# Optimization experiments

Hardware: AMD Instinct MI355X
Metric: run time of the kernel (lower is better)

## Reference

```python
import jax, jax.numpy as jnp
import numpy as np

B, N, E, H = 8, 2048, 1024, 16
D = E // H

def setup_inputs() -> dict:
    key = jax.random.key(0)
    kx, kw1, kb1, kw2, kb2 = jax.random.split(key, 5)
    scale = 0.02
    return {
        "x": jax.random.normal(kx, (B, N, E), dtype=jnp.float32),
        "Wqkv": jax.random.normal(kw1, (3 * E, E), dtype=jnp.float32) * scale,
        "bqkv": jax.random.normal(kb1, (3 * E,), dtype=jnp.float32) * scale,
        "Wo": jax.random.normal(kw2, (E, E), dtype=jnp.float32) * scale,
        "bo": jax.random.normal(kb2, (E,), dtype=jnp.float32) * scale,
    }

def reference(x, Wqkv, bqkv, Wo, bo):
    b, n, e = x.shape
    h, d = H, D
    # qkv projection: torch Linear is x @ W.T + b
    qkv = x @ Wqkv.T + bqkv                                   # [B,N,3E]
    qkv = qkv.reshape(b, n, 3, h, d).transpose(2, 0, 3, 1, 4)  # [3,B,H,N,D]
    q, k, v = qkv[0], qkv[1], qkv[2]                           # each [B,H,N,D]
    # NOTE: replicates the original's einsum labeling exactly: with q,k of
    # shape [B,H,N,D], 'nqhd,nkhd->nhqk' contracts over D and yields [B,N,H,H]
    # (softmax over the head axis), matching the torch source bit-for-bit.
    energy = jnp.einsum('nqhd,nkhd->nhqk', q, k)               # [B,N,H,H]
    attention = jax.nn.softmax(energy / jnp.sqrt(jnp.float32(e)), axis=-1)
    out = jnp.einsum('nhql,nlhd->nqhd', attention, v)          # [B,H,N,D]
    out = out.reshape(b, n, e)                                 # same raw-buffer reshape as torch
    return out @ Wo.T + bo
```

## Files before the change

### kernel.cpp

```cpp
#include <hip/hip_runtime.h>
#include <hip/hip_bf16.h>
#include <stdint.h>


typedef __attribute__((ext_vector_type(8))) short short8;
typedef __attribute__((ext_vector_type(8))) unsigned short ushort8;
typedef __attribute__((ext_vector_type(4))) float floatx4;

__device__ __forceinline__ unsigned short f2bf(float f) {
  union { float f; uint32_t u; } x; x.f = f;
  uint32_t u = x.u;
  return (unsigned short)((u + 0x7fffu + ((u >> 16) & 1u)) >> 16);
}
__device__ __forceinline__ float bf2f(unsigned short s) {
  union { uint32_t u; float f; } x; x.u = ((uint32_t)s) << 16; return x.f;
}
__device__ __forceinline__ void unpack8(uint4 u, float* f) {
  f[0] = bf2f((unsigned short)(u.x & 0xffffu)); f[1] = bf2f((unsigned short)(u.x >> 16));
  f[2] = bf2f((unsigned short)(u.y & 0xffffu)); f[3] = bf2f((unsigned short)(u.y >> 16));
  f[4] = bf2f((unsigned short)(u.z & 0xffffu)); f[5] = bf2f((unsigned short)(u.z >> 16));
  f[6] = bf2f((unsigned short)(u.w & 0xffffu)); f[7] = bf2f((unsigned short)(u.w >> 16));
}

__global__ __launch_bounds__(256) void cvt_all(const float* __restrict__ x,
                                               const float* __restrict__ w1,
                                               const float* __restrict__ w2,
                                               unsigned short* __restrict__ xb,
                                               unsigned short* __restrict__ w1b,
                                               unsigned short* __restrict__ w2b) {
  int i = blockIdx.x * 256 + threadIdx.x;
  const float* src;
  unsigned short* dst;
  if (i < 2097152) {
    src = x; dst = xb;
  } else if (i < 2097152 + 393216) {
    i -= 2097152; src = w1; dst = w1b;
  } else {
    i -= 2490368; src = w2; dst = w2b;
  }
  long base = (long)i * 8;
  const float4* p = (const float4*)(src + base);
  float4 a = p[0], b = p[1];
  ushort8 r;
  r[0] = f2bf(a.x); r[1] = f2bf(a.y); r[2] = f2bf(a.z); r[3] = f2bf(a.w);
  r[4] = f2bf(b.x); r[5] = f2bf(b.y); r[6] = f2bf(b.z); r[7] = f2bf(b.w);
  *(ushort8*)(dst + base) = r;
}

__device__ __forceinline__ void gl2lds16(const void* g, void* l) {
  __builtin_amdgcn_global_load_lds(
      (const uint32_t __attribute__((address_space(1)))*)g,
      (uint32_t __attribute__((address_space(3)))*)(uint32_t)(uintptr_t)l,
      16, 0, 0);
}

template <bool OUT_BF16>
__device__ __forceinline__ void gemm256_core(const unsigned short* __restrict__ A,
                                             const unsigned short* __restrict__ Bm,
                                             const float* __restrict__ bias,
                                             void* __restrict__ Cout,
                                             int K, int ncols, int ldc) {
  __shared__ __align__(16) char lds[131072];
  char* lA = lds;
  char* lB = lds + 65536;

  const int id = blockIdx.x;
  const int local = id % (8 * ncols);
  const int brow = (id / (8 * ncols)) * 8 + (local & 7);
  const int bcol = local >> 3;
  const long row0 = (long)brow * 256;
  const long col0 = (long)bcol * 256;

  const int tid = threadIdx.x;
  const int lane = tid & 63;
  const int wave = tid >> 6;
  const int wm = wave >> 2;
  const int wn = wave & 3;
  const int l15 = lane & 15;
  const int lk = lane >> 4;

  float bv[4];
#pragma unroll
  for (int n = 0; n < 4; ++n) bv[n] = bias[col0 + wn * 64 + n * 16 + l15];
  asm volatile("s_waitcnt vmcnt(0)" ::: "memory");

  const int trow = tid >> 2;
  const int gch = (tid & 3) ^ ((tid >> 3) & 3);
  const unsigned short* gA = A + (row0 + trow) * (long)K + gch * 8;
  const unsigned short* gB = Bm + (col0 + trow) * (long)K + gch * 8;
  const long rstep = (long)128 * K;
  char* dA = lA + tid * 16;
  char* dB = lB + tid * 16;

  const int ch = ((lk ^ ((l15 >> 1) & 3)) << 4);
  const int aoff = (wm * 128 + l15) * 64 + ch;
  const int boff = (wn * 64 + l15) * 64 + ch;

  floatx4 acc[8][4] = {};
  const int NT = K >> 5;

#pragma unroll
  for (int t = 0; t < 3; ++t) {
    const long ko = (long)t * 32;
    gl2lds16(gA + ko, dA + t * 16384);
    gl2lds16(gA + rstep + ko, dA + t * 16384 + 8192);
    gl2lds16(gB + ko, dB + t * 16384);
    gl2lds16(gB + rstep + ko, dB + t * 16384 + 8192);
  }
  asm volatile("s_waitcnt vmcnt(8)" ::: "memory");
  __builtin_amdgcn_s_barrier();

#pragma unroll 1
  for (int kt = 0; kt < NT; ++kt) {
    const char* bufA = lA + (kt & 3) * 16384;
    const char* bufB = lB + (kt & 3) * 16384;
    const bool stage = (kt + 3 < NT);
    const long ko = (long)(kt + 3) * 32;
    const int sb = ((kt + 3) & 3) * 16384;

    short8 af[8], bfr[4];
#pragma unroll
    for (int n = 0; n < 4; ++n) bfr[n] = *(const short8*)(bufB + boff + n * 1024);
    af[0] = *(const short8*)(bufA + aoff + 0 * 1024);
    af[1] = *(const short8*)(bufA + aoff + 1 * 1024);
    af[2] = *(const short8*)(bufA + aoff + 2 * 1024);
    af[3] = *(const short8*)(bufA + aoff + 3 * 1024);
    asm volatile("s_waitcnt lgkmcnt(2)" ::: "memory");
    __builtin_amdgcn_sched_barrier(0);
    __builtin_amdgcn_s_setprio(1);
#pragma unroll
    for (int n = 0; n < 4; ++n) {
      acc[0][n] = __builtin_amdgcn_mfma_f32_16x16x32_bf16(af[0], bfr[n], acc[0][n], 0, 0, 0);
      acc[1][n] = __builtin_amdgcn_mfma_f32_16x16x32_bf16(af[1], bfr[n], acc[1][n], 0, 0, 0);
    }
    __builtin_amdgcn_s_setprio(0);
    af[4] = *(const short8*)(bufA + aoff + 4 * 1024);
    af[5] = *(const short8*)(bufA + aoff + 5 * 1024);
    asm volatile("s_waitcnt lgkmcnt(2)" ::: "memory");
    __builtin_amdgcn_sched_barrier(0);
    __builtin_amdgcn_s_setprio(1);
#pragma unroll
    for (int n = 0; n < 4; ++n) {
      acc[2][n] = __builtin_amdgcn_mfma_f32_16x16x32_bf16(af[2], bfr[n], acc[2][n], 0, 0, 0);
      acc[3][n] = __builtin_amdgcn_mfma_f32_16x16x32_bf16(af[3], bfr[n], acc[3][n], 0, 0, 0);
    }
    __builtin_amdgcn_s_setprio(0);
    af[6] = *(const short8*)(bufA + aoff + 6 * 1024);
    af[7] = *(const short8*)(bufA + aoff + 7 * 1024);
    if (stage) {
      gl2lds16(gA + ko, dA + sb);
      gl2lds16(gA + rstep + ko, dA + sb + 8192);
      gl2lds16(gB + ko, dB + sb);
      gl2lds16(gB + rstep + ko, dB + sb + 8192);
    }
    asm volatile("s_waitcnt lgkmcnt(2)" ::: "memory");
    __builtin_amdgcn_sched_barrier(0);
    __builtin_amdgcn_s_setprio(1);
#pragma unroll
    for (int n = 0; n < 4; ++n) {
      acc[4][n] = __builtin_amdgcn_mfma_f32_16x16x32_bf16(af[4], bfr[n], acc[4][n], 0, 0, 0);
      acc[5][n] = __builtin_amdgcn_mfma_f32_16x16x32_bf16(af[5], bfr[n], acc[5][n], 0, 0, 0);
    }
    __builtin_amdgcn_s_setprio(0);
    asm volatile("s_waitcnt lgkmcnt(0)" ::: "memory");
    __builtin_amdgcn_sched_barrier(0);
    __builtin_amdgcn_s_setprio(1);
#pragma unroll
    for (int n = 0; n < 4; ++n) {
      acc[6][n] = __builtin_amdgcn_mfma_f32_16x16x32_bf16(af[6], bfr[n], acc[6][n], 0, 0, 0);
      acc[7][n] = __builtin_amdgcn_mfma_f32_16x16x32_bf16(af[7], bfr[n], acc[7][n], 0, 0, 0);
    }
    __builtin_amdgcn_s_setprio(0);
    __builtin_amdgcn_sched_barrier(0);
    if (kt < NT - 3) { asm volatile("s_waitcnt vmcnt(8)" ::: "memory"); }
    else if (kt == NT - 3) { asm volatile("s_waitcnt vmcnt(4)" ::: "memory"); }
    else if (kt == NT - 2) { asm volatile("s_waitcnt vmcnt(0)" ::: "memory"); }
    __builtin_amdgcn_s_barrier();
  }

  const long crow0 = row0 + wm * 128 + lk * 4;
  const long ccol0 = col0 + wn * 64 + l15;
#pragma unroll
  for (int m = 0; m < 8; ++m)
#pragma unroll
    for (int n = 0; n < 4; ++n)
#pragma unroll
      for (int r = 0; r < 4; ++r) {
        const long row = crow0 + m * 16 + r;
        const long col = ccol0 + n * 16;
        const float v = acc[m][n][r] + bv[n];
        if (OUT_BF16)
          ((unsigned short*)Cout)[row * ldc + col] = f2bf(v);
        else
          ((float*)Cout)[row * ldc + col] = v;
      }
}

__global__ __launch_bounds__(512, 2) void gemm_qkv(const unsigned short* __restrict__ A,
                                                   const unsigned short* __restrict__ Bm,
                                                   const float* __restrict__ bias,
                                                   unsigned short* __restrict__ Cout, int K) {
  gemm256_core<true>(A, Bm, bias, Cout, K, 12, 3072);
}
__global__ __launch_bounds__(512, 2) void gemm_out(const unsigned short* __restrict__ A,
                                                   const unsigned short* __restrict__ Bm,
                                                   const float* __restrict__ bias,
                                                   float* __restrict__ Cout, int K) {
  gemm256_core<false>(A, Bm, bias, Cout, K, 4, 1024);
}

__global__ __launch_bounds__(256) void attn_kernel(const unsigned short* __restrict__ qkv,
                                                   unsigned short* __restrict__ out2) {
  __shared__ __align__(16) char lds[4 * 6144];
  const int tid = threadIdx.x;
  const int wave = tid >> 6;
  const int lane = tid & 63;
  const int token = blockIdx.x * 4 + wave;
  const int head = lane >> 2;
  const int sub = lane & 3;
  const int b = token >> 11;
  const int s = token & 2047;

  const char* gbase = (const char*)qkv + (long)token * 6144;
  char* lbase = lds + wave * 6144;
#pragma unroll
  for (int p = 0; p < 6; p++)
    gl2lds16(gbase + p * 1024 + lane * 16, lbase + p * 1024 + lane * 16);
  __syncthreads();

  float qf[16];
  {
    const uint4* qp = (const uint4*)(lbase + head * 128 + sub * 32);
    unpack8(qp[0], qf);
    unpack8(qp[1], qf + 8);
  }

  float e[16];
  const char* kbase = lbase + 2048 + sub * 32;
  for (int j = 0; j < 16; j++) {
    const uint4* kp = (const uint4*)(kbase + j * 128);
    float kf[16];
    unpack8(kp[0], kf);
    unpack8(kp[1], kf + 8);
    float a0 = 0.f, a1 = 0.f, a2 = 0.f, a3 = 0.f;
#pragma unroll
    for (int c = 0; c < 4; c++) {
      a0 += qf[c] * kf[c];
      a1 += qf[c + 4] * kf[c + 4];
      a2 += qf[c + 8] * kf[c + 8];
      a3 += qf[c + 12] * kf[c + 12];
    }
    float ej = (a0 + a1) + (a2 + a3);
    ej += __shfl_xor(ej, 1);
    ej += __shfl_xor(ej, 2);
    e[j] = ej * 0.03125f;
  }

  float mx = e[0];
#pragma unroll
  for (int j = 1; j < 16; j++) mx = fmaxf(mx, e[j]);
  float sum = 0.f;
#pragma unroll
  for (int j = 0; j < 16; j++) { e[j] = __expf(e[j] - mx); sum += e[j]; }
  const float inv = 1.f / sum;

  float o[16];
#pragma unroll
  for (int d = 0; d < 16; d++) o[d] = 0.f;
  const char* vbase = lbase + 4096 + sub * 32;
  for (int j = 0; j < 16; j++) {
    const float wgt = e[j] * inv;
    const uint4* vp = (const uint4*)(vbase + j * 128);
    float vf[16];
    unpack8(vp[0], vf);
    unpack8(vp[1], vf + 8);
#pragma unroll
    for (int d = 0; d < 16; d++) o[d] += wgt * vf[d];
  }

  const long row = (long)b * 2048 + head * 128 + (s >> 4);
  unsigned short* op = out2 + row * 1024 + (long)(s & 15) * 64 + sub * 16;
#pragma unroll
  for (int w = 0; w < 2; w++) {
    ushort8 r;
#pragma unroll
    for (int c = 0; c < 8; c++) r[c] = f2bf(o[w * 8 + c]);
    *(ushort8*)(op + w * 8) = r;
  }
}

extern "C" void kernel_launch(void* const* d_in, const int* in_sizes, int n_in,
                              void* d_out, int out_size, void* d_ws, size_t ws_size,
                              hipStream_t stream) {
  const float* x    = (const float*)d_in[0];
  const float* Wqkv = (const float*)d_in[1];
  const float* bqkv = (const float*)d_in[2];
  const float* Wo   = (const float*)d_in[3];
  const float* bo   = (const float*)d_in[4];
  float* out = (float*)d_out;

  char* ws = (char*)d_ws;
  unsigned short* x_bf    = (unsigned short*)(ws);
  unsigned short* wqkv_bf = (unsigned short*)(ws + 33554432);
  unsigned short* wo_bf   = (unsigned short*)(ws + 39845888);
  unsigned short* qkv_bf  = (unsigned short*)(ws + 41943040);
  unsigned short* out2_bf = (unsigned short*)(ws + 142606336);

  cvt_all<<<10240, 256, 0, stream>>>(x, Wqkv, Wo, x_bf, wqkv_bf, wo_bf);

  gemm_qkv<<<64 * 12, 512, 0, stream>>>(x_bf, wqkv_bf, bqkv, qkv_bf, 1024);

  attn_kernel<<<4096, 256, 0, stream>>>(qkv_bf, out2_bf);

  gemm_out<<<64 * 4, 512, 0, stream>>>(out2_bf, wo_bf, bo, out, 1024);
}
```

Baseline: 316.0 us.

## Compute head-mixing attention with bf16 MFMA and XOR-swizzled LDS layout

Replaces the scalar per-lane dot products and weighted sums in the attention kernel with 16x16x32 bf16 MFMA instructions for both QK^T and attention×V. An XOR swizzle is applied when staging qkv rows into LDS to avoid bank conflicts on the transposed reads. Attention probabilities are now rounded to bf16 before the PV product, which adds precision loss. The V operand is gathered with scalar 16-bit LDS reads, and half the MFMA K dimension is zero-padded.

```diff
diff --git a/kernel.cpp b/kernel.cpp
--- a/kernel.cpp
+++ b/kernel.cpp
@@ -5,21 +5,13 @@
 
 typedef __attribute__((ext_vector_type(8))) short short8;
 typedef __attribute__((ext_vector_type(8))) unsigned short ushort8;
+typedef __attribute__((ext_vector_type(4))) unsigned short ushort4v;
 typedef __attribute__((ext_vector_type(4))) float floatx4;
 
 __device__ __forceinline__ unsigned short f2bf(float f) {
   union { float f; uint32_t u; } x; x.f = f;
   uint32_t u = x.u;
   return (unsigned short)((u + 0x7fffu + ((u >> 16) & 1u)) >> 16);
-}
-__device__ __forceinline__ float bf2f(unsigned short s) {
-  union { uint32_t u; float f; } x; x.u = ((uint32_t)s) << 16; return x.f;
-}
-__device__ __forceinline__ void unpack8(uint4 u, float* f) {
-  f[0] = bf2f((unsigned short)(u.x & 0xffffu)); f[1] = bf2f((unsigned short)(u.x >> 16));
-  f[2] = bf2f((unsigned short)(u.y & 0xffffu)); f[3] = bf2f((unsigned short)(u.y >> 16));
-  f[4] = bf2f((unsigned short)(u.z & 0xffffu)); f[5] = bf2f((unsigned short)(u.z >> 16));
-  f[6] = bf2f((unsigned short)(u.w & 0xffffu)); f[7] = bf2f((unsigned short)(u.w >> 16));
 }
 
 __global__ __launch_bounds__(256) void cvt_all(const float* __restrict__ x,
@@ -216,76 +208,82 @@
   const int wave = tid >> 6;
   const int lane = tid & 63;
   const int token = blockIdx.x * 4 + wave;
-  const int head = lane >> 2;
-  const int sub = lane & 3;
+  const int l15 = lane & 15;
+  const int lk = lane >> 4;
   const int b = token >> 11;
   const int s = token & 2047;
 
   const char* gbase = (const char*)qkv + (long)token * 6144;
   char* lbase = lds + wave * 6144;
 #pragma unroll
-  for (int p = 0; p < 6; p++)
-    gl2lds16(gbase + p * 1024 + lane * 16, lbase + p * 1024 + lane * 16);
+  for (int p = 0; p < 6; p++) {
+    const int o = p * 1024 + lane * 16;
+    const int row = o >> 7;
+    const int chs = ((o >> 4) & 7) ^ (row & 7);
+    const int src = (o & ~127) | (chs << 4);
+    gl2lds16(gbase + src, lbase + o);
+  }
   __syncthreads();
 
-  float qf[16];
-  {
-    const uint4* qp = (const uint4*)(lbase + head * 128 + sub * 32);
-    unpack8(qp[0], qf);
-    unpack8(qp[1], qf + 8);
-  }
-
-  float e[16];
-  const char* kbase = lbase + 2048 + sub * 32;
-  for (int j = 0; j < 16; j++) {
-    const uint4* kp = (const uint4*)(kbase + j * 128);
-    float kf[16];
-    unpack8(kp[0], kf);
-    unpack8(kp[1], kf + 8);
-    float a0 = 0.f, a1 = 0.f, a2 = 0.f, a3 = 0.f;
-#pragma unroll
-    for (int c = 0; c < 4; c++) {
-      a0 += qf[c] * kf[c];
-      a1 += qf[c + 4] * kf[c + 4];
-      a2 += qf[c + 8] * kf[c + 8];
-      a3 += qf[c + 12] * kf[c + 12];
-    }
-    float ej = (a0 + a1) + (a2 + a3);
-    ej += __shfl_xor(ej, 1);
-    ej += __shfl_xor(ej, 2);
-    e[j] = ej * 0.03125f;
-  }
-
-  float mx = e[0];
-#pragma unroll
-  for (int j = 1; j < 16; j++) mx = fmaxf(mx, e[j]);
+  const int sw = l15 & 7;
+  const char* qrow = lbase + l15 * 128;
+  const char* krow = lbase + 2048 + l15 * 128;
+  const short8 kf0 = *(const short8*)(krow + ((lk ^ sw) << 4));
+  const short8 kf1 = *(const short8*)(krow + (((lk + 4) ^ sw) << 4));
+  const short8 qf0 = *(const short8*)(qrow + ((lk ^ sw) << 4));
+  const short8 qf1 = *(const short8*)(qrow + (((lk + 4) ^ sw) << 4));
+  floatx4 e = {};
+  e = __builtin_amdgcn_mfma_f32_16x16x32_bf16(kf0, qf0, e, 0, 0, 0);
+  e = __builtin_amdgcn_mfma_f32_16x16x32_bf16(kf1, qf1, e, 0, 0, 0);
+
+  float ev[4];
+#pragma unroll
+  for (int r = 0; r < 4; ++r) ev[r] = e[r] * 0.03125f;
+  float mx = fmaxf(fmaxf(ev[0], ev[1]), fmaxf(ev[2], ev[3]));
+  mx = fmaxf(mx, __shfl_xor(mx, 16));
+  mx = fmaxf(mx, __shfl_xor(mx, 32));
   float sum = 0.f;
 #pragma unroll
-  for (int j = 0; j < 16; j++) { e[j] = __expf(e[j] - mx); sum += e[j]; }
+  for (int r = 0; r < 4; ++r) { ev[r] = __expf(ev[r] - mx); sum += ev[r]; }
+  sum += __shfl_xor(sum, 16);
+  sum += __shfl_xor(sum, 32);
   const float inv = 1.f / sum;
 
-  float o[16];
-#pragma unroll
-  for (int d = 0; d < 16; d++) o[d] = 0.f;
-  const char* vbase = lbase + 4096 + sub * 32;
-  for (int j = 0; j < 16; j++) {
-    const float wgt = e[j] * inv;
-    const uint4* vp = (const uint4*)(vbase + j * 128);
-    float vf[16];
-    unpack8(vp[0], vf);
-    unpack8(vp[1], vf + 8);
-#pragma unroll
-    for (int d = 0; d < 16; d++) o[d] += wgt * vf[d];
-  }
-
-  const long row = (long)b * 2048 + head * 128 + (s >> 4);
-  unsigned short* op = out2 + row * 1024 + (long)(s & 15) * 64 + sub * 16;
-#pragma unroll
-  for (int w = 0; w < 2; w++) {
-    ushort8 r;
-#pragma unroll
-    for (int c = 0; c < 8; c++) r[c] = f2bf(o[w * 8 + c]);
-    *(ushort8*)(op + w * 8) = r;
+  const uint32_t pa = (uint32_t)f2bf(ev[0] * inv) | ((uint32_t)f2bf(ev[1] * inv) << 16);
+  const uint32_t pb = (uint32_t)f2bf(ev[2] * inv) | ((uint32_t)f2bf(ev[3] * inv) << 16);
+  const int src0 = (l15 + 32 * lk) & 63;
+  uint32_t w0 = __shfl(pa, src0);
+  uint32_t w1 = __shfl(pb, src0);
+  uint32_t w2 = __shfl(pa, (src0 + 16) & 63);
+  uint32_t w3 = __shfl(pb, (src0 + 16) & 63);
+  if (lk >= 2) { w0 = 0; w1 = 0; w2 = 0; w3 = 0; }
+  union { short8 s8; uint32_t u[4]; } attf;
+  attf.u[0] = w0; attf.u[1] = w1; attf.u[2] = w2; attf.u[3] = w3;
+
+  const long orow = (long)b * 2048 + l15 * 128 + (s >> 4);
+  unsigned short* op = out2 + orow * 1024 + (long)(s & 15) * 64;
+#pragma unroll
+  for (int c = 0; c < 4; ++c) {
+    union { short8 s8; unsigned short us[8]; } vf;
+    if (lk < 2) {
+      const int byte_in = (c * 16 + l15) * 2;
+#pragma unroll
+      for (int i = 0; i < 8; ++i) {
+        const int j = lk * 8 + i;
+        const int chv = ((byte_in >> 4) ^ (j & 7));
+        vf.us[i] = *(const unsigned short*)(lbase + 4096 + j * 128 + (chv << 4) +
+                                            (byte_in & 15));
+      }
+    } else {
+#pragma unroll
+      for (int i = 0; i < 8; ++i) vf.us[i] = 0;
+    }
+    floatx4 o = {};
+    o = __builtin_amdgcn_mfma_f32_16x16x32_bf16(vf.s8, attf.s8, o, 0, 0, 0);
+    ushort4v r4;
+#pragma unroll
+    for (int r = 0; r < 4; ++r) r4[r] = f2bf(o[r]);
+    *(ushort4v*)(op + c * 16 + lk * 4) = r4;
   }
 }
 
```

Result: faster. 302.3 us (-4.3%).
